# Kernel optimization log

Measured on AMD Instinct MI355X. Metric: run time of the kernel, lower is better.

## Reference

```python
import jax, jax.numpy as jnp
import numpy as np

B, T, C, H, L, V = 64, 256, 256, 8, 6, 96
EPS = 1e-5


def _layernorm(x, w, b):
    m = x.mean(-1, keepdims=True)
    v = x.var(-1, keepdims=True)
    return (x - m) / jnp.sqrt(v + EPS) * w + b


def setup_inputs() -> dict:
    key = jax.random.key(0)
    ks = jax.random.split(key, 16)
    s = 0.05
    n = lambda k, sh: jax.random.normal(k, sh, jnp.float32) * s
    return {
        'idx': jax.random.randint(ks[0], (B, T), 0, V),
        'target': jax.random.randint(ks[1], (B, T), 0, V),
        'tok_emb': n(ks[2], (V, C)),
        'pos_emb': n(ks[3], (T, C)),
        'Wq': n(ks[4], (L, C, C)),
        'Wk': n(ks[5], (L, C, C)),
        'Wv': n(ks[6], (L, C, C)),
        'Wo': n(ks[7], (L, C, C)),
        'bo': jnp.zeros((L, C), jnp.float32),
        'W1': n(ks[8], (L, C, C)),
        'b1': jnp.zeros((L, C), jnp.float32),
        'W2': n(ks[9], (L, C, C)),
        'b2': jnp.zeros((L, C), jnp.float32),
        'ln1_w': jnp.ones((L, C), jnp.float32),
        'ln1_b': jnp.zeros((L, C), jnp.float32),
        'ln2_w': jnp.ones((L, C), jnp.float32),
        'ln2_b': jnp.zeros((L, C), jnp.float32),
        'lnf_w': jnp.ones((C,), jnp.float32),
        'lnf_b': jnp.zeros((C,), jnp.float32),
        'Wlm': n(ks[10], (C, V)),
        'blm': jnp.zeros((V,), jnp.float32),
    }


def _forward(idx, target, tok_emb, pos_emb, Wq, Wk, Wv, Wo, bo, W1, b1, W2, b2,
             ln1_w, ln1_b, ln2_w, ln2_b, lnf_w, lnf_b, Wlm, blm):
    Bc, Tc = idx.shape
    hs = C // H
    scale = C ** (-0.5)  # NOTE: original scales by n_embed**-0.5, not head_size**-0.5
    x = tok_emb[idx] + pos_emb[:Tc]              # [B,T,C]
    causal = jnp.tril(jnp.ones((Tc, Tc), bool))  # [T,T]
    for l in range(L):
        q = (x @ Wq[l]).reshape(Bc, Tc, H, hs)
        k = (x @ Wk[l]).reshape(Bc, Tc, H, hs)
        v = (x @ Wv[l]).reshape(Bc, Tc, H, hs)
        w = jnp.einsum('bqhd,bkhd->bhqk', q, k) * scale
        w = jnp.where(causal, w, -jnp.inf)
        w = jax.nn.softmax(w, axis=-1)
        att = jnp.einsum('bhqk,bkhd->bqhd', w, v).reshape(Bc, Tc, C)
        x = _layernorm(x + att @ Wo[l] + bo[l], ln1_w[l], ln1_b[l])  # post-residual LN
        h = jax.nn.relu(x @ W1[l] + b1[l]) @ W2[l] + b2[l]
        x = _layernorm(x + h, ln2_w[l], ln2_b[l])
    x = _layernorm(x, lnf_w, lnf_b)
    logits = (x @ Wlm + blm).reshape(Bc * Tc, V)
    logp = jax.nn.log_softmax(logits, axis=-1)
    nll = -jnp.take_along_axis(logp, target.reshape(-1, 1), axis=1)
    loss = nll.mean()
    return logits, loss


def reference(idx, target, tok_emb, pos_emb, Wq, Wk, Wv, Wo, bo, W1, b1, W2, b2,
              ln1_w, ln1_b, ln2_w, ln2_b, lnf_w, lnf_b, Wlm, blm):
    return _forward(idx, target, tok_emb, pos_emb, Wq, Wk, Wv, Wo, bo, W1, b1, W2, b2,
                    ln1_w, ln1_b, ln2_w, ln2_b, lnf_w, lnf_b, Wlm, blm)
```

## Files before the change

### kernel.cpp

```cpp
#include <hip/hip_runtime.h>

typedef unsigned short u16;

#define NT   16384
#define CDIM 256
#define LAYERS 6

using bf16x8 = __attribute__((ext_vector_type(8))) __bf16;
using f32x4  = __attribute__((ext_vector_type(4))) float;

__device__ __forceinline__ u16 f2bf(float x){
  unsigned u = __float_as_uint(x);
  u += 0x7fffu + ((u >> 16) & 1u);
  return (u16)(u >> 16);
}

__device__ __forceinline__ void gll16(const u16* g, u16* l){
  __builtin_amdgcn_global_load_lds(
      (const __attribute__((address_space(1))) unsigned int*)g,
      (__attribute__((address_space(3))) unsigned int*)l, 16, 0, 0);
}

__global__ __launch_bounds__(256) void wconv_k(
    const float* __restrict__ Wq, const float* __restrict__ Wk,
    const float* __restrict__ Wv, const float* __restrict__ Wo,
    const float* __restrict__ W1, const float* __restrict__ W2,
    const float* __restrict__ Wlm, u16* __restrict__ WT)
{
  __shared__ float tile[64][65];
  const int z = blockIdx.z;
  const float* src; u16* dst; int N = 256, Npad = 256;
  if (z < 18){
    const int l = z / 3, which = z % 3;
    const float* a[3] = {Wq, Wk, Wv};
    src = a[which] + (size_t)l * 65536;
    dst = WT + (size_t)l * 196608 + (size_t)which * 65536;
  } else if (z < 36){
    const int i = z - 18, j = i / 6, l = i % 6;
    const float* a[3] = {Wo, W1, W2};
    src = a[j] + (size_t)l * 65536;
    dst = WT + 1179648 + (size_t)(j * 6 + l) * 65536;
  } else {
    src = Wlm; dst = WT + 2359296; N = 96; Npad = 128;
  }
  const int n0 = blockIdx.y * 64, k0 = blockIdx.x * 64;
  if (n0 >= Npad) return;
  const int c = threadIdx.x & 63, r0 = threadIdx.x >> 6;
  #pragma unroll
  for (int i = 0; i < 16; ++i){
    const int r = r0 + i * 4;
    tile[r][c] = (n0 + c < N) ? src[(size_t)(k0 + r) * N + n0 + c] : 0.f;
  }
  __syncthreads();
  #pragma unroll
  for (int i = 0; i < 16; ++i){
    const int cp = r0 + i * 4;
    dst[(size_t)(n0 + cp) * CDIM + k0 + c] = f2bf(tile[c][cp]);
  }
}

__global__ __launch_bounds__(256) void embed_k(
    const int* __restrict__ idx, const float* __restrict__ tok,
    const float* __restrict__ pos, float* __restrict__ X, u16* __restrict__ Xb)
{
  const int w = threadIdx.x >> 6, l = threadIdx.x & 63;
  const int r = blockIdx.x * 4 + w;
  const int id = idx[r];
  float4 tv = *reinterpret_cast<const float4*>(tok + (size_t)id * CDIM + l * 4);
  float4 pv = *reinterpret_cast<const float4*>(pos + (size_t)(r & 255) * CDIM + l * 4);
  float4 y = {tv.x + pv.x, tv.y + pv.y, tv.z + pv.z, tv.w + pv.w};
  *reinterpret_cast<float4*>(X + (size_t)r * CDIM + l * 4) = y;
  union { u16 u[4]; uint2 q; } p;
  p.u[0] = f2bf(y.x); p.u[1] = f2bf(y.y); p.u[2] = f2bf(y.z); p.u[3] = f2bf(y.w);
  *reinterpret_cast<uint2*>(Xb + (size_t)r * CDIM + l * 4) = p.q;
}

template<int TM, bool BIAS, bool RELU, bool RES, bool OBF>
__global__ __launch_bounds__(256) void gemm_k(
    const u16* __restrict__ A, const u16* __restrict__ WT,
    const float* __restrict__ bias, const float* __restrict__ res,
    void* __restrict__ outp, int N, int ldo)
{
  __shared__ u16 As[TM * 64];
  __shared__ u16 Bs[128 * 64];
  const int t = threadIdx.x, l = t & 63, w = t >> 6;
  const int wr = w >> 1, wc = w & 1;
  const int m0 = blockIdx.x * TM, n0 = blockIdx.y * 128;
  const int lr = l & 15, lk = (l >> 4) * 8;
  const int row = t >> 3, c8 = (t & 7) * 8;
  constexpr int MR = TM / 32;
  f32x4 acc[MR][4] = {};

  for (int kt = 0; kt < 4; ++kt){
    const int k0 = kt * 64;
    if (kt) __syncthreads();
    #pragma unroll
    for (int i = 0; i < MR; ++i)
      gll16(A + (size_t)(m0 + row + 32 * i) * CDIM + k0 + c8, As + t * 8 + i * 2048);
    #pragma unroll
    for (int i = 0; i < 4; ++i)
      gll16(WT + (size_t)(n0 + row + 32 * i) * CDIM + k0 + c8, Bs + t * 8 + i * 2048);
    __syncthreads();
    #pragma unroll
    for (int kk = 0; kk < 64; kk += 32){
      bf16x8 af[MR], bfr[4];
      #pragma unroll
      for (int m = 0; m < MR; ++m)
        af[m] = *reinterpret_cast<const bf16x8*>(&As[(wr * (TM / 2) + m * 16 + lr) * 64 + kk + lk]);
      #pragma unroll
      for (int n = 0; n < 4; ++n)
        bfr[n] = *reinterpret_cast<const bf16x8*>(&Bs[(wc * 64 + n * 16 + lr) * 64 + kk + lk]);
      #pragma unroll
      for (int m = 0; m < MR; ++m)
        #pragma unroll
        for (int n = 0; n < 4; ++n)
          acc[m][n] = __builtin_amdgcn_mfma_f32_16x16x32_bf16(af[m], bfr[n], acc[m][n], 0, 0, 0);
    }
  }

  const int rj = (l >> 4) * 4;
  #pragma unroll
  for (int m = 0; m < MR; ++m){
    #pragma unroll
    for (int n = 0; n < 4; ++n){
      const int gcol = n0 + wc * 64 + n * 16 + lr;
      if (gcol < N){
        #pragma unroll
        for (int j = 0; j < 4; ++j){
          const int grow = m0 + wr * (TM / 2) + m * 16 + rj + j;
          const size_t o = (size_t)grow * ldo + gcol;
          float v = acc[m][n][j];
          if (BIAS) v += bias[gcol];
          if (RES)  v += res[o];
          if (RELU) v = fmaxf(v, 0.f);
          if (OBF) ((u16*)outp)[o] = f2bf(v);
          else     ((float*)outp)[o] = v;
        }
      }
    }
  }
}

__global__ __launch_bounds__(256) void attn_k(
    const u16* __restrict__ QKV, u16* __restrict__ O)
{
  __shared__ u16 Vt[32][264];
  __shared__ u16 Ps[64][264];
  const int bh = blockIdx.x, b = bh >> 3, h = bh & 7;
  const size_t rbase = (size_t)b * 256 * 768;
  const int qc = h * 32, kc = 256 + h * 32, vc = 512 + h * 32;
  const int t = threadIdx.x, l = t & 63, w = t >> 6;
  const int lr = l & 15, lk = (l >> 4) * 8;

  {
    const uint4* vp = reinterpret_cast<const uint4*>(QKV + rbase + (size_t)t * 768 + vc);
    #pragma unroll
    for (int i = 0; i < 4; ++i){
      union { uint4 q; u16 u[8]; } p; p.q = vp[i];
      #pragma unroll
      for (int j = 0; j < 8; ++j) Vt[i * 8 + j][t] = p.u[j];
    }
  }
  bf16x8 kf[16];
  #pragma unroll
  for (int n = 0; n < 16; ++n)
    kf[n] = *reinterpret_cast<const bf16x8*>(QKV + rbase + (size_t)(n * 16 + lr) * 768 + kc + lk);
  __syncthreads();

  for (int c = 0; c < 4; ++c){
    const int rowb = c * 64 + w * 16;
    bf16x8 qa = *reinterpret_cast<const bf16x8*>(QKV + rbase + (size_t)(rowb + lr) * 768 + qc + lk);

    f32x4 s[16];
    #pragma unroll
    for (int n = 0; n < 16; ++n){
      f32x4 z = {};
      s[n] = __builtin_amdgcn_mfma_f32_16x16x32_bf16(qa, kf[n], z, 0, 0, 0);
    }

    float inv[4];
    const int prow = w * 16 + (l >> 4) * 4;
    #pragma unroll
    for (int j = 0; j < 4; ++j){
      const int qrow = rowb + (l >> 4) * 4 + j;
      float sv[16]; float mx = -1e30f;
      #pragma unroll
      for (int n = 0; n < 16; ++n){
        float vv = s[n][j] * 0.0625f;
        sv[n] = ((n * 16 + lr) <= qrow) ? vv : -1e30f;
        mx = fmaxf(mx, sv[n]);
      }
      #pragma unroll
      for (int o = 1; o < 16; o <<= 1) mx = fmaxf(mx, __shfl_xor(mx, o));
      float sum = 0.f;
      #pragma unroll
      for (int n = 0; n < 16; ++n){
        float p = __expf(sv[n] - mx);
        sum += p;
        Ps[prow + j][n * 16 + lr] = f2bf(p);
      }
      #pragma unroll
      for (int o = 1; o < 16; o <<= 1) sum += __shfl_xor(sum, o);
      inv[j] = 1.f / sum;
    }
    __syncthreads();

    f32x4 o0 = {}, o1 = {};
    #pragma unroll
    for (int kc2 = 0; kc2 < 8; ++kc2){
      bf16x8 pa = *reinterpret_cast<const bf16x8*>(&Ps[w * 16 + lr][kc2 * 32 + lk]);
      bf16x8 v0 = *reinterpret_cast<const bf16x8*>(&Vt[lr][kc2 * 32 + lk]);
      bf16x8 v1 = *reinterpret_cast<const bf16x8*>(&Vt[16 + lr][kc2 * 32 + lk]);
      o0 = __builtin_amdgcn_mfma_f32_16x16x32_bf16(pa, v0, o0, 0, 0, 0);
      o1 = __builtin_amdgcn_mfma_f32_16x16x32_bf16(pa, v1, o1, 0, 0, 0);
    }
    #pragma unroll
    for (int j = 0; j < 4; ++j){
      const int qrow = rowb + (l >> 4) * 4 + j;
      u16* op = O + (size_t)(b * 256 + qrow) * CDIM + h * 32;
      op[lr]      = f2bf(o0[j] * inv[j]);
      op[16 + lr] = f2bf(o1[j] * inv[j]);
    }
    __syncthreads();
  }
}

template<bool WX>
__global__ __launch_bounds__(256) void ln_k(
    const float* __restrict__ in, const float* __restrict__ w,
    const float* __restrict__ b, float* __restrict__ X, u16* __restrict__ Xb)
{
  const int wv = threadIdx.x >> 6, l = threadIdx.x & 63;
  const int r = blockIdx.x * 4 + wv;
  float4 v = *reinterpret_cast<const float4*>(in + (size_t)r * CDIM + l * 4);
  float s = v.x + v.y + v.z + v.w;
  float q = v.x * v.x + v.y * v.y + v.z * v.z + v.w * v.w;
  #pragma unroll
  for (int o = 32; o; o >>= 1){ s += __shfl_xor(s, o); q += __shfl_xor(q, o); }
  const float mean = s * (1.f / 256.f);
  const float var  = q * (1.f / 256.f) - mean * mean;
  const float rstd = rsqrtf(var + 1e-5f);
  float4 w4 = *reinterpret_cast<const float4*>(w + l * 4);
  float4 b4 = *reinterpret_cast<const float4*>(b + l * 4);
  float4 y;
  y.x = (v.x - mean) * rstd * w4.x + b4.x;
  y.y = (v.y - mean) * rstd * w4.y + b4.y;
  y.z = (v.z - mean) * rstd * w4.z + b4.z;
  y.w = (v.w - mean) * rstd * w4.w + b4.w;
  if (WX) *reinterpret_cast<float4*>(X + (size_t)r * CDIM + l * 4) = y;
  union { u16 u[4]; uint2 q2; } p;
  p.u[0] = f2bf(y.x); p.u[1] = f2bf(y.y); p.u[2] = f2bf(y.z); p.u[3] = f2bf(y.w);
  *reinterpret_cast<uint2*>(Xb + (size_t)r * CDIM + l * 4) = p.q2;
}

__global__ __launch_bounds__(256) void nll_k(
    const float* __restrict__ logits, const int* __restrict__ target,
    float* __restrict__ nll)
{
  const int w = threadIdx.x >> 6, l = threadIdx.x & 63;
  const int r = blockIdx.x * 4 + w;
  const float* row = logits + (size_t)r * 96;
  float v0 = row[l];
  float v1 = (l < 32) ? row[64 + l] : -1e30f;
  float m = fmaxf(v0, v1);
  #pragma unroll
  for (int o = 32; o; o >>= 1) m = fmaxf(m, __shfl_xor(m, o));
  float s = __expf(v0 - m) + ((l < 32) ? __expf(v1 - m) : 0.f);
  #pragma unroll
  for (int o = 32; o; o >>= 1) s += __shfl_xor(s, o);
  if (l == 0) nll[r] = logf(s) + m - row[target[r]];
}

__global__ __launch_bounds__(256) void loss_k(
    const float* __restrict__ nll, float* __restrict__ out)
{
  __shared__ float rs[4];
  float s = 0.f;
  for (int i = threadIdx.x; i < NT; i += 256) s += nll[i];
  #pragma unroll
  for (int o = 32; o; o >>= 1) s += __shfl_xor(s, o);
  if ((threadIdx.x & 63) == 0) rs[threadIdx.x >> 6] = s;
  __syncthreads();
  if (threadIdx.x == 0) out[0] = (rs[0] + rs[1] + rs[2] + rs[3]) * (1.f / 16384.f);
}

extern "C" void kernel_launch(void* const* d_in, const int* in_sizes, int n_in,
                              void* d_out, int out_size, void* d_ws, size_t ws_size,
                              hipStream_t stream)
{
  const int*   idx    = (const int*)  d_in[0];
  const int*   target = (const int*)  d_in[1];
  const float* tok    = (const float*)d_in[2];
  const float* pos    = (const float*)d_in[3];
  const float* Wq     = (const float*)d_in[4];
  const float* Wk     = (const float*)d_in[5];
  const float* Wv     = (const float*)d_in[6];
  const float* Wo     = (const float*)d_in[7];
  const float* bo     = (const float*)d_in[8];
  const float* W1     = (const float*)d_in[9];
  const float* b1     = (const float*)d_in[10];
  const float* W2     = (const float*)d_in[11];
  const float* b2     = (const float*)d_in[12];
  const float* ln1w   = (const float*)d_in[13];
  const float* ln1b   = (const float*)d_in[14];
  const float* ln2w   = (const float*)d_in[15];
  const float* ln2b   = (const float*)d_in[16];
  const float* lnfw   = (const float*)d_in[17];
  const float* lnfb   = (const float*)d_in[18];
  const float* Wlm    = (const float*)d_in[19];
  const float* blm    = (const float*)d_in[20];
  float* out = (float*)d_out;

  char* ws = (char*)d_ws;
  float* X   = (float*)(ws);
  float* y   = (float*)(ws + (16u << 20));
  u16*   Xb  = (u16*)  (ws + (32u << 20));
  u16*   QKV = (u16*)  (ws + (40u << 20));
  u16*   O   = (u16*)  (ws + (64u << 20));
  u16*   hB  = (u16*)  (ws + (72u << 20));
  u16*   WT  = (u16*)  (ws + (80u << 20));
  float* nl  = (float*)(ws + (88u << 20));

  wconv_k<<<dim3(4, 4, 37), 256, 0, stream>>>(Wq, Wk, Wv, Wo, W1, W2, Wlm, WT);
  embed_k<<<NT / 4, 256, 0, stream>>>(idx, tok, pos, X, Xb);

  for (int l = 0; l < LAYERS; ++l){
    const u16* wqkv = WT + (size_t)l * 196608;
    const u16* wo   = WT + 1179648 + (size_t)(0 * 6 + l) * 65536;
    const u16* w1   = WT + 1179648 + (size_t)(1 * 6 + l) * 65536;
    const u16* w2   = WT + 1179648 + (size_t)(2 * 6 + l) * 65536;

    gemm_k<128, false, false, false, true><<<dim3(128, 6), 256, 0, stream>>>(
        Xb, wqkv, nullptr, nullptr, QKV, 768, 768);
    attn_k<<<512, 256, 0, stream>>>(QKV, O);
    gemm_k<64, true, false, true, false><<<dim3(256, 2), 256, 0, stream>>>(
        O, wo, bo + l * 256, X, y, 256, 256);
    ln_k<true><<<NT / 4, 256, 0, stream>>>(y, ln1w + l * 256, ln1b + l * 256, X, Xb);
    gemm_k<64, true, true, false, true><<<dim3(256, 2), 256, 0, stream>>>(
        Xb, w1, b1 + l * 256, nullptr, hB, 256, 256);
    gemm_k<64, true, false, true, false><<<dim3(256, 2), 256, 0, stream>>>(
        hB, w2, b2 + l * 256, X, y, 256, 256);
    ln_k<true><<<NT / 4, 256, 0, stream>>>(y, ln2w + l * 256, ln2b + l * 256, X, Xb);
  }

  ln_k<false><<<NT / 4, 256, 0, stream>>>(X, lnfw, lnfb, nullptr, Xb);
  gemm_k<64, true, false, false, false><<<dim3(256, 1), 256, 0, stream>>>(
      Xb, WT + 2359296, blm, nullptr, out, 96, 96);
  nll_k<<<NT / 4, 256, 0, stream>>>(out, target, nl);
  loss_k<<<1, 256, 0, stream>>>(nl, out + (size_t)NT * 96);
}
```

Baseline: 665.1 us.

## Fuse residual LayerNorm into full-row GEMM epilogues with double-buffered K tiles

The GEMM kernel is generalized over tile shape and warp layout. The Wo and W2 projections now use 64x256 full-row tiles, so the epilogue can add bias and residual and then apply LayerNorm in place. Row sums are reduced with shuffles plus shared memory, and both fp32 X and bf16 Xb are written. This removes two standalone LN launches per layer along with the fp32 y round trip, and double-buffered LDS staging overlaps loads with MFMA. The cost is fewer blocks (256 instead of 512) and more LDS and registers per block, which may lower occupancy. The residual is read from X and written back to X in the same kernel, which is safe only because each block owns whole rows.

```diff
diff --git a/kernel.cpp b/kernel.cpp
--- a/kernel.cpp
+++ b/kernel.cpp
@@ -75,66 +75,139 @@
   *reinterpret_cast<uint2*>(Xb + (size_t)r * CDIM + l * 4) = p.q;
 }
 
-template<int TM, bool BIAS, bool RELU, bool RES, bool OBF>
+template<int TM, int TN, int WR, int WC, bool DBUF,
+         bool BIAS, bool RELU, bool RES, bool LN, bool OBF>
 __global__ __launch_bounds__(256) void gemm_k(
     const u16* __restrict__ A, const u16* __restrict__ WT,
     const float* __restrict__ bias, const float* __restrict__ res,
-    void* __restrict__ outp, int N, int ldo)
-{
-  __shared__ u16 As[TM * 64];
-  __shared__ u16 Bs[128 * 64];
+    void* __restrict__ outp, u16* __restrict__ out2,
+    const float* __restrict__ lnw, const float* __restrict__ lnb,
+    int N, int ldo)
+{
+  constexpr int NB = DBUF ? 2 : 1;
+  constexpr int MR = TM / WR / 16, NR = TN / WC / 16;
+  __shared__ u16 As[NB * TM * 64];
+  __shared__ u16 Bs[NB * TN * 64];
   const int t = threadIdx.x, l = t & 63, w = t >> 6;
-  const int wr = w >> 1, wc = w & 1;
-  const int m0 = blockIdx.x * TM, n0 = blockIdx.y * 128;
+  const int wr = w / WC, wc = w % WC;
+  const int m0 = blockIdx.x * TM, n0 = blockIdx.y * TN;
   const int lr = l & 15, lk = (l >> 4) * 8;
-  const int row = t >> 3, c8 = (t & 7) * 8;
-  constexpr int MR = TM / 32;
-  f32x4 acc[MR][4] = {};
-
-  for (int kt = 0; kt < 4; ++kt){
+  const int srow = t >> 3, sc8 = (t & 7) * 8;
+  const int rb = wr * (TM / WR), cb = wc * (TN / WC);
+  f32x4 acc[MR][NR] = {};
+
+  auto stage = [&](int buf, int kt){
     const int k0 = kt * 64;
-    if (kt) __syncthreads();
-    #pragma unroll
-    for (int i = 0; i < MR; ++i)
-      gll16(A + (size_t)(m0 + row + 32 * i) * CDIM + k0 + c8, As + t * 8 + i * 2048);
-    #pragma unroll
-    for (int i = 0; i < 4; ++i)
-      gll16(WT + (size_t)(n0 + row + 32 * i) * CDIM + k0 + c8, Bs + t * 8 + i * 2048);
-    __syncthreads();
+    u16* as = As + buf * (TM * 64);
+    u16* bs = Bs + buf * (TN * 64);
+    #pragma unroll
+    for (int i = 0; i < TM / 32; ++i)
+      gll16(A + (size_t)(m0 + srow + 32 * i) * CDIM + k0 + sc8, as + i * 2048 + t * 8);
+    #pragma unroll
+    for (int i = 0; i < TN / 32; ++i)
+      gll16(WT + (size_t)(n0 + srow + 32 * i) * CDIM + k0 + sc8, bs + i * 2048 + t * 8);
+  };
+  auto compute = [&](int buf){
+    const u16* as = As + buf * (TM * 64);
+    const u16* bs = Bs + buf * (TN * 64);
     #pragma unroll
     for (int kk = 0; kk < 64; kk += 32){
-      bf16x8 af[MR], bfr[4];
+      bf16x8 af[MR], bf[NR];
       #pragma unroll
       for (int m = 0; m < MR; ++m)
-        af[m] = *reinterpret_cast<const bf16x8*>(&As[(wr * (TM / 2) + m * 16 + lr) * 64 + kk + lk]);
-      #pragma unroll
-      for (int n = 0; n < 4; ++n)
-        bfr[n] = *reinterpret_cast<const bf16x8*>(&Bs[(wc * 64 + n * 16 + lr) * 64 + kk + lk]);
+        af[m] = *reinterpret_cast<const bf16x8*>(&as[(rb + m * 16 + lr) * 64 + kk + lk]);
+      #pragma unroll
+      for (int n = 0; n < NR; ++n)
+        bf[n] = *reinterpret_cast<const bf16x8*>(&bs[(cb + n * 16 + lr) * 64 + kk + lk]);
       #pragma unroll
       for (int m = 0; m < MR; ++m)
         #pragma unroll
-        for (int n = 0; n < 4; ++n)
-          acc[m][n] = __builtin_amdgcn_mfma_f32_16x16x32_bf16(af[m], bfr[n], acc[m][n], 0, 0, 0);
+        for (int n = 0; n < NR; ++n)
+          acc[m][n] = __builtin_amdgcn_mfma_f32_16x16x32_bf16(af[m], bf[n], acc[m][n], 0, 0, 0);
+    }
+  };
+
+  if constexpr (DBUF){
+    stage(0, 0);
+    __syncthreads();
+    #pragma unroll
+    for (int kt = 0; kt < 4; ++kt){
+      if (kt < 3) stage((kt + 1) & 1, kt + 1);
+      compute(kt & 1);
+      if (kt < 3) __syncthreads();
+    }
+  } else {
+    #pragma unroll
+    for (int kt = 0; kt < 4; ++kt){
+      if (kt) __syncthreads();
+      stage(0, kt);
+      __syncthreads();
+      compute(0);
     }
   }
 
   const int rj = (l >> 4) * 4;
-  #pragma unroll
-  for (int m = 0; m < MR; ++m){
-    #pragma unroll
-    for (int n = 0; n < 4; ++n){
-      const int gcol = n0 + wc * 64 + n * 16 + lr;
-      if (gcol < N){
+  if constexpr (LN){
+    __shared__ float redS[TM][WC + 1], redQ[TM][WC + 1];
+    #pragma unroll
+    for (int m = 0; m < MR; ++m){
+      #pragma unroll
+      for (int j = 0; j < 4; ++j){
+        const int lrow = rb + m * 16 + rj + j;
+        const int grow = m0 + lrow;
+        float s = 0.f, q = 0.f;
         #pragma unroll
-        for (int j = 0; j < 4; ++j){
-          const int grow = m0 + wr * (TM / 2) + m * 16 + rj + j;
-          const size_t o = (size_t)grow * ldo + gcol;
-          float v = acc[m][n][j];
-          if (BIAS) v += bias[gcol];
-          if (RES)  v += res[o];
-          if (RELU) v = fmaxf(v, 0.f);
-          if (OBF) ((u16*)outp)[o] = f2bf(v);
-          else     ((float*)outp)[o] = v;
+        for (int n = 0; n < NR; ++n){
+          const int gcol = cb + n * 16 + lr;
+          float v = acc[m][n][j] + bias[gcol] + res[(size_t)grow * CDIM + gcol];
+          acc[m][n][j] = v;
+          s += v; q += v * v;
+        }
+        #pragma unroll
+        for (int o = 1; o < 16; o <<= 1){ s += __shfl_xor(s, o); q += __shfl_xor(q, o); }
+        if (lr == 0){ redS[lrow][wc] = s; redQ[lrow][wc] = q; }
+      }
+    }
+    __syncthreads();
+    #pragma unroll
+    for (int m = 0; m < MR; ++m){
+      #pragma unroll
+      for (int j = 0; j < 4; ++j){
+        const int lrow = rb + m * 16 + rj + j;
+        const int grow = m0 + lrow;
+        float s = 0.f, q = 0.f;
+        #pragma unroll
+        for (int c = 0; c < WC; ++c){ s += redS[lrow][c]; q += redQ[lrow][c]; }
+        const float mean = s * (1.f / 256.f);
+        const float rstd = rsqrtf(q * (1.f / 256.f) - mean * mean + 1e-5f);
+        #pragma unroll
+        for (int n = 0; n < NR; ++n){
+          const int gcol = cb + n * 16 + lr;
+          const size_t o = (size_t)grow * CDIM + gcol;
+          const float y = (acc[m][n][j] - mean) * rstd * lnw[gcol] + lnb[gcol];
+          ((float*)outp)[o] = y;
+          out2[o] = f2bf(y);
+        }
+      }
+    }
+  } else {
+    #pragma unroll
+    for (int m = 0; m < MR; ++m){
+      #pragma unroll
+      for (int n = 0; n < NR; ++n){
+        const int gcol = n0 + cb + n * 16 + lr;
+        if (gcol < N){
+          #pragma unroll
+          for (int j = 0; j < 4; ++j){
+            const int grow = m0 + rb + m * 16 + rj + j;
+            const size_t o = (size_t)grow * ldo + gcol;
+            float v = acc[m][n][j];
+            if (BIAS) v += bias[gcol];
+            if (RES)  v += res[o];
+            if (RELU) v = fmaxf(v, 0.f);
+            if (OBF) ((u16*)outp)[o] = f2bf(v);
+            else     ((float*)outp)[o] = v;
+          }
         }
       }
     }
@@ -225,10 +298,9 @@
   }
 }
 
-template<bool WX>
 __global__ __launch_bounds__(256) void ln_k(
     const float* __restrict__ in, const float* __restrict__ w,
-    const float* __restrict__ b, float* __restrict__ X, u16* __restrict__ Xb)
+    const float* __restrict__ b, u16* __restrict__ Xb)
 {
   const int wv = threadIdx.x >> 6, l = threadIdx.x & 63;
   const int r = blockIdx.x * 4 + wv;
@@ -242,14 +314,11 @@
   const float rstd = rsqrtf(var + 1e-5f);
   float4 w4 = *reinterpret_cast<const float4*>(w + l * 4);
   float4 b4 = *reinterpret_cast<const float4*>(b + l * 4);
-  float4 y;
-  y.x = (v.x - mean) * rstd * w4.x + b4.x;
-  y.y = (v.y - mean) * rstd * w4.y + b4.y;
-  y.z = (v.z - mean) * rstd * w4.z + b4.z;
-  y.w = (v.w - mean) * rstd * w4.w + b4.w;
-  if (WX) *reinterpret_cast<float4*>(X + (size_t)r * CDIM + l * 4) = y;
   union { u16 u[4]; uint2 q2; } p;
-  p.u[0] = f2bf(y.x); p.u[1] = f2bf(y.y); p.u[2] = f2bf(y.z); p.u[3] = f2bf(y.w);
+  p.u[0] = f2bf((v.x - mean) * rstd * w4.x + b4.x);
+  p.u[1] = f2bf((v.y - mean) * rstd * w4.y + b4.y);
+  p.u[2] = f2bf((v.z - mean) * rstd * w4.z + b4.z);
+  p.u[3] = f2bf((v.w - mean) * rstd * w4.w + b4.w);
   *reinterpret_cast<uint2*>(Xb + (size_t)r * CDIM + l * 4) = p.q2;
 }
 
@@ -307,21 +376,20 @@
   const float* ln2b   = (const float*)d_in[16];
   const float* lnfw   = (const float*)d_in[17];
   const float* lnfb   = (const float*)d_in[18];
-  const float* Wlm    = (const float*)d_in[19];
   const float* blm    = (const float*)d_in[20];
   float* out = (float*)d_out;
 
   char* ws = (char*)d_ws;
   float* X   = (float*)(ws);
-  float* y   = (float*)(ws + (16u << 20));
-  u16*   Xb  = (u16*)  (ws + (32u << 20));
-  u16*   QKV = (u16*)  (ws + (40u << 20));
-  u16*   O   = (u16*)  (ws + (64u << 20));
-  u16*   hB  = (u16*)  (ws + (72u << 20));
-  u16*   WT  = (u16*)  (ws + (80u << 20));
-  float* nl  = (float*)(ws + (88u << 20));
-
-  wconv_k<<<dim3(4, 4, 37), 256, 0, stream>>>(Wq, Wk, Wv, Wo, W1, W2, Wlm, WT);
+  u16*   Xb  = (u16*)  (ws + (16u << 20));
+  u16*   QKV = (u16*)  (ws + (24u << 20));
+  u16*   O   = (u16*)  (ws + (48u << 20));
+  u16*   hB  = (u16*)  (ws + (56u << 20));
+  u16*   WT  = (u16*)  (ws + (64u << 20));
+  float* nl  = (float*)(ws + (72u << 20));
+
+  wconv_k<<<dim3(4, 4, 37), 256, 0, stream>>>(Wq, Wk, Wv, Wo, W1, W2,
+                                              (const float*)d_in[19], WT);
   embed_k<<<NT / 4, 256, 0, stream>>>(idx, tok, pos, X, Xb);
 
   for (int l = 0; l < LAYERS; ++l){
@@ -330,22 +398,25 @@
     const u16* w1   = WT + 1179648 + (size_t)(1 * 6 + l) * 65536;
     const u16* w2   = WT + 1179648 + (size_t)(2 * 6 + l) * 65536;
 
-    gemm_k<128, false, false, false, true><<<dim3(128, 6), 256, 0, stream>>>(
-        Xb, wqkv, nullptr, nullptr, QKV, 768, 768);
+    gemm_k<128, 128, 2, 2, false, false, false, false, false, true>
+        <<<dim3(128, 6), 256, 0, stream>>>(
+        Xb, wqkv, nullptr, nullptr, QKV, nullptr, nullptr, nullptr, 768, 768);
     attn_k<<<512, 256, 0, stream>>>(QKV, O);
-    gemm_k<64, true, false, true, false><<<dim3(256, 2), 256, 0, stream>>>(
-        O, wo, bo + l * 256, X, y, 256, 256);
-    ln_k<true><<<NT / 4, 256, 0, stream>>>(y, ln1w + l * 256, ln1b + l * 256, X, Xb);
-    gemm_k<64, true, true, false, true><<<dim3(256, 2), 256, 0, stream>>>(
-        Xb, w1, b1 + l * 256, nullptr, hB, 256, 256);
-    gemm_k<64, true, false, true, false><<<dim3(256, 2), 256, 0, stream>>>(
-        hB, w2, b2 + l * 256, X, y, 256, 256);
-    ln_k<true><<<NT / 4, 256, 0, stream>>>(y, ln2w + l * 256, ln2b + l * 256, X, Xb);
-  }
-
-  ln_k<false><<<NT / 4, 256, 0, stream>>>(X, lnfw, lnfb, nullptr, Xb);
-  gemm_k<64, true, false, false, false><<<dim3(256, 1), 256, 0, stream>>>(
-      Xb, WT + 2359296, blm, nullptr, out, 96, 96);
+    gemm_k<64, 256, 1, 4, true, true, false, true, true, false>
+        <<<dim3(256, 1), 256, 0, stream>>>(
+        O, wo, bo + l * 256, X, X, Xb, ln1w + l * 256, ln1b + l * 256, 256, 256);
+    gemm_k<64, 256, 1, 4, true, true, true, false, false, true>
+        <<<dim3(256, 1), 256, 0, stream>>>(
+        Xb, w1, b1 + l * 256, nullptr, hB, nullptr, nullptr, nullptr, 256, 256);
+    gemm_k<64, 256, 1, 4, true, true, false, true, true, false>
+        <<<dim3(256, 1), 256, 0, stream>>>(
+        hB, w2, b2 + l * 256, X, X, Xb, ln2w + l * 256, ln2b + l * 256, 256, 256);
+  }
+
+  ln_k<<<NT / 4, 256, 0, stream>>>(X, lnfw, lnfb, Xb);
+  gemm_k<64, 128, 2, 2, true, true, false, false, false, false>
+      <<<dim3(256, 1), 256, 0, stream>>>(
+      Xb, WT + 2359296, blm, nullptr, out, nullptr, nullptr, nullptr, 96, 96);
   nll_k<<<NT / 4, 256, 0, stream>>>(out, target, nl);
   loss_k<<<1, 256, 0, stream>>>(nl, out + (size_t)NT * 96);
 }
```

New measurement: 667.9 us. No clear change (+0.4%).
